# Kernel tuning notes

Measured on AMD Instinct MI355X. Metric: run time of the kernel, lower is better.

## Reference

```python
import jax, jax.numpy as jnp
import numpy as np

V_TH = 1.0
V_RESET = 0.0
ALPHA = 4.0  # sigmoid surrogate sharpness used by the Triton backward kernel


@jax.custom_vjp
def spike_fn(over_th):
    # Heaviside forward; sigmoid surrogate gradient in backward.
    return (over_th >= 0).astype(over_th.dtype)


def _spike_fwd(over_th):
    return spike_fn(over_th), over_th


def _spike_bwd(over_th, g):
    sig = jax.nn.sigmoid(ALPHA * over_th)
    return (g * (1.0 - sig) * sig * ALPHA,)


spike_fn.defvjp(_spike_fwd, _spike_bwd)


def setup_inputs() -> dict:
    key = jax.random.key(0)
    k1, _ = jax.random.split(key)
    T, B, D = 32, 128, 8192
    x_seq = jax.random.normal(k1, (T, B, D), dtype=jnp.float32)
    v_init = jnp.zeros((B, D), dtype=jnp.float32)  # module init: v = v_reset = 0.0
    return {"x_seq": x_seq, "v_init": v_init}


def reference(x_seq, v_init):
    # IF neuron, multi-step, hard reset:
    #   h_t   = x_t + v_{t-1}
    #   s_t   = H(h_t - v_th)
    #   v_t   = h_t * (1 - s_t) + v_reset * s_t
    def step(v, x):
        h = x + v
        s = spike_fn(h - V_TH)
        v_next = h * (1.0 - s) + V_RESET * s
        return v_next, s

    _, spike_seq = jax.lax.scan(step, v_init, x_seq)
    return spike_seq
```

## Files before the change

### kernel.cpp

```cpp
#include <hip/hip_runtime.h>


typedef float v2f __attribute__((ext_vector_type(2)));

template <int T, int C>
__global__ __launch_bounds__(256) void if_node_multicol(
    const float* __restrict__ x,
    const float* __restrict__ v0,
    float* __restrict__ out,
    long q)
{
    long i = (long)blockIdx.x * blockDim.x + threadIdx.x;
    if (i >= q) return;

    const v2f* __restrict__ x2 = (const v2f*)x;
    v2f*       __restrict__ o2 = (v2f*)out;
    const v2f* __restrict__ vv = (const v2f*)v0;

    const long n2 = q * C;

    v2f v[C];
#pragma unroll
    for (int c = 0; c < C; ++c)
        v[c] = vv[i + (long)c * q];

#pragma unroll
    for (int t = 0; t < T; ++t) {
        v2f xv[C];
#pragma unroll
        for (int c = 0; c < C; ++c)
            xv[c] = x2[(long)t * n2 + i + (long)c * q];
#pragma unroll
        for (int c = 0; c < C; ++c) {
            float hx = xv[c].x + v[c].x;
            float hy = xv[c].y + v[c].y;
            bool sx = (hx - 1.0f) >= 0.0f;
            bool sy = (hy - 1.0f) >= 0.0f;
            v2f s;
            s.x = sx ? 1.0f : 0.0f;
            s.y = sy ? 1.0f : 0.0f;
            v[c].x = sx ? 0.0f : hx;
            v[c].y = sy ? 0.0f : hy;
            __builtin_nontemporal_store(s, &o2[(long)t * n2 + i + (long)c * q]);
        }
    }
}

__global__ __launch_bounds__(256) void if_node_f2_generic(
    const float* __restrict__ x, const float* __restrict__ v0,
    float* __restrict__ out, long n2, int T)
{
    long i = (long)blockIdx.x * blockDim.x + threadIdx.x;
    if (i >= n2) return;
    const v2f* x2 = (const v2f*)x;
    v2f*       o2 = (v2f*)out;
    v2f v = ((const v2f*)v0)[i];
    for (int t = 0; t < T; ++t) {
        v2f xv = x2[(long)t * n2 + i];
        float hx = xv.x + v.x;
        float hy = xv.y + v.y;
        bool sx = (hx - 1.0f) >= 0.0f;
        bool sy = (hy - 1.0f) >= 0.0f;
        v2f s;
        s.x = sx ? 1.0f : 0.0f;
        s.y = sy ? 1.0f : 0.0f;
        v.x = sx ? 0.0f : hx;
        v.y = sy ? 0.0f : hy;
        o2[(long)t * n2 + i] = s;
    }
}

__global__ __launch_bounds__(256) void if_node_scalar(
    const float* __restrict__ x, const float* __restrict__ v0,
    float* __restrict__ out, long n, int T)
{
    long i = (long)blockIdx.x * blockDim.x + threadIdx.x;
    if (i >= n) return;
    float v = v0[i];
    for (int t = 0; t < T; ++t) {
        float h = x[(long)t * n + i] + v;
        bool s = (h - 1.0f) >= 0.0f;
        out[(long)t * n + i] = s ? 1.0f : 0.0f;
        v = s ? 0.0f : h;
    }
}

extern "C" void kernel_launch(void* const* d_in, const int* in_sizes, int n_in,
                              void* d_out, int out_size, void* d_ws, size_t ws_size,
                              hipStream_t stream) {
    const float* x  = (const float*)d_in[0];
    const float* v0 = (const float*)d_in[1];
    float* out = (float*)d_out;

    long n = in_sizes[1];
    int  T = (int)(in_sizes[0] / n);

    int block = 256;
    constexpr int C = 4;
    if (T == 32 && (n % (2 * C)) == 0) {
        long n2 = n >> 1;
        long q  = n2 / C;
        long grid = (q + block - 1) / block;
        if_node_multicol<32, C><<<dim3((unsigned)grid), dim3(block), 0, stream>>>(
            x, v0, out, q);
    } else if ((n & 1) == 0) {
        long n2 = n >> 1;
        long grid = (n2 + block - 1) / block;
        if_node_f2_generic<<<dim3((unsigned)grid), dim3(block), 0, stream>>>(
            x, v0, out, n2, T);
    } else {
        long grid = (n + block - 1) / block;
        if_node_scalar<<<dim3((unsigned)grid), dim3(block), 0, stream>>>(
            x, v0, out, n, T);
    }
}
```

Measured before the change: 230.9 us.

## Bitpack spikes in registers and prefetch next timestep inputs

Records each column's spike history as 32-bit masks during the recurrence and writes all outputs in a separate pass after the loads. Loads for timestep t+1 are issued before computing timestep t using a register double buffer. This aims to separate read and write traffic and keep more loads in flight. It adds unpacking work, and the compiler may already have been scheduling loads similarly in the fully unrolled loop.

```diff
diff --git a/kernel.cpp b/kernel.cpp
--- a/kernel.cpp
+++ b/kernel.cpp
@@ -4,12 +4,13 @@
 typedef float v2f __attribute__((ext_vector_type(2)));
 
 template <int T, int C>
-__global__ __launch_bounds__(256) void if_node_multicol(
+__global__ __launch_bounds__(256) void if_node_bitpack(
     const float* __restrict__ x,
     const float* __restrict__ v0,
     float* __restrict__ out,
     long q)
 {
+    static_assert(T <= 32, "bitmask is 32-bit");
     long i = (long)blockIdx.x * blockDim.x + threadIdx.x;
     if (i >= q) return;
 
@@ -20,27 +21,47 @@
     const long n2 = q * C;
 
     v2f v[C];
+    unsigned mx[C], my[C];
+#pragma unroll
+    for (int c = 0; c < C; ++c) {
+        v[c] = vv[i + (long)c * q];
+        mx[c] = 0u;
+        my[c] = 0u;
+    }
+
+    v2f buf[2][C];
 #pragma unroll
     for (int c = 0; c < C; ++c)
-        v[c] = vv[i + (long)c * q];
+        buf[0][c] = x2[i + (long)c * q];
 
 #pragma unroll
     for (int t = 0; t < T; ++t) {
-        v2f xv[C];
+        const int cur = t & 1;
+        if (t + 1 < T) {
 #pragma unroll
-        for (int c = 0; c < C; ++c)
-            xv[c] = x2[(long)t * n2 + i + (long)c * q];
+            for (int c = 0; c < C; ++c)
+                buf[cur ^ 1][c] = x2[(long)(t + 1) * n2 + i + (long)c * q];
+        }
 #pragma unroll
         for (int c = 0; c < C; ++c) {
-            float hx = xv[c].x + v[c].x;
-            float hy = xv[c].y + v[c].y;
+            float hx = buf[cur][c].x + v[c].x;
+            float hy = buf[cur][c].y + v[c].y;
             bool sx = (hx - 1.0f) >= 0.0f;
             bool sy = (hy - 1.0f) >= 0.0f;
-            v2f s;
-            s.x = sx ? 1.0f : 0.0f;
-            s.y = sy ? 1.0f : 0.0f;
+            mx[c] |= sx ? (1u << t) : 0u;
+            my[c] |= sy ? (1u << t) : 0u;
             v[c].x = sx ? 0.0f : hx;
             v[c].y = sy ? 0.0f : hy;
+        }
+    }
+
+#pragma unroll
+    for (int t = 0; t < T; ++t) {
+#pragma unroll
+        for (int c = 0; c < C; ++c) {
+            v2f s;
+            s.x = ((mx[c] >> t) & 1u) ? 1.0f : 0.0f;
+            s.y = ((my[c] >> t) & 1u) ? 1.0f : 0.0f;
             __builtin_nontemporal_store(s, &o2[(long)t * n2 + i + (long)c * q]);
         }
     }
@@ -101,7 +122,7 @@
         long n2 = n >> 1;
         long q  = n2 / C;
         long grid = (q + block - 1) / block;
-        if_node_multicol<32, C><<<dim3((unsigned)grid), dim3(block), 0, stream>>>(
+        if_node_bitpack<32, C><<<dim3((unsigned)grid), dim3(block), 0, stream>>>(
             x, v0, out, q);
     } else if ((n & 1) == 0) {
         long n2 = n >> 1;
```

New measurement: 232.6 us. About the same (+0.7%).
